# Kernel tuning notes

Hardware: AMD Instinct MI355X
Metric: run time of the kernel (lower is better)

The kernel has to match this reference:

```python
import jax, jax.numpy as jnp
import numpy as np

NUM_HEADS = 4
WS = 3


def setup_inputs() -> dict:
    key = jax.random.key(0)
    k1, k2, k3 = jax.random.split(key, 3)
    B, Hs, Ws_, C = 16, 96, 96, 256
    x = jax.random.normal(k1, (B, Hs * Ws_, C), dtype=jnp.float32)
    # torch nn.Linear weights: [out_features, in_features]
    Wqkv = jax.random.normal(k2, (3 * C, C), dtype=jnp.float32) * (1.0 / np.sqrt(C))
    Wproj = jax.random.normal(k3, (C, C), dtype=jnp.float32) * (1.0 / np.sqrt(C))
    return {"x": x, "Wqkv": Wqkv, "Wproj": Wproj, "H": Hs, "W": Ws_}


def reference(x, Wqkv, Wproj, H, W):
    B, N, C = x.shape
    ws = WS
    nh = NUM_HEADS
    hd = C // nh
    scale = hd ** -0.5

    pad_h = (ws - H % ws) % ws
    pad_w = (ws - W % ws) % ws
    xg = x.reshape(B, H, W, C)
    if pad_h > 0 or pad_w > 0:
        xg = jnp.pad(xg, ((0, 0), (0, pad_h), (0, pad_w), (0, 0)))
    H_pad, W_pad = H + pad_h, W + pad_w
    nWh, nWw = H_pad // ws, W_pad // ws
    Bw = B * nWh * nWw

    # window partition: [B, nWh, ws, nWw, ws, C] -> [Bw, ws*ws, C]
    xw = xg.reshape(B, nWh, ws, nWw, ws, C).transpose(0, 1, 3, 2, 4, 5)
    xw = xw.reshape(Bw, ws * ws, C)

    # qkv projection (Linear, no bias): x @ W^T
    qkv = xw @ Wqkv.T                                   # [Bw, 9, 3C]
    qkv = qkv.reshape(Bw, ws * ws, 3, nh, hd).transpose(2, 0, 3, 1, 4)
    q, k, v = qkv[0], qkv[1], qkv[2]                    # [Bw, nh, 9, hd]

    attn = jnp.einsum("bhqd,bhkd->bhqk", q, k) * scale  # [Bw, nh, 9, 9]
    attn = jax.nn.softmax(attn, axis=-1)
    out = jnp.einsum("bhqk,bhkd->bhqd", attn, v)        # [Bw, nh, 9, hd]
    out = out.transpose(0, 2, 1, 3).reshape(Bw, ws * ws, C)
    out = out @ Wproj.T

    # window unpartition
    out = out.reshape(B, nWh, nWw, ws, ws, C).transpose(0, 1, 3, 2, 4, 5)
    out = out.reshape(B, H_pad, W_pad, C)
    if pad_h > 0 or pad_w > 0:
        out = out[:, :H, :W, :]
    return out.reshape(B, H * W, C)
```

## Files before the change

kernel.cpp:

```cpp
#include <hip/hip_runtime.h>
#include <hip/hip_bf16.h>

using f32x4  = __attribute__((ext_vector_type(4))) float;
using bf16x8 = __attribute__((ext_vector_type(8))) short;
using bf16x4 = __attribute__((ext_vector_type(4))) short;
using u32x2  = __attribute__((ext_vector_type(2))) unsigned int;
using u32x4  = __attribute__((ext_vector_type(4))) unsigned int;

__device__ __forceinline__ float bf2f(short s) {
    unsigned u = ((unsigned)(unsigned short)s) << 16;
    return __builtin_bit_cast(float, u);
}
__device__ __forceinline__ unsigned short f2b(float f) {
    unsigned u = __builtin_bit_cast(unsigned, f);
    unsigned r = u + 0x7FFFu + ((u >> 16) & 1u);
    return (unsigned short)(r >> 16);
}
__device__ __forceinline__ void gl_lds16(const void* g, void* l) {
    __builtin_amdgcn_global_load_lds((const __attribute__((address_space(1))) void*)g,
                                     (__attribute__((address_space(3))) void*)l, 16, 0, 0);
}

__global__ void k_wconv(const float* __restrict__ wq, const float* __restrict__ wp,
                        unsigned short* __restrict__ out) {
    int i = blockIdx.x * 256 + threadIdx.x;
    float v = (i < 196608) ? wq[i] : wp[i - 196608];
    out[i] = f2b(v);
}

__global__ __launch_bounds__(256) void k_qkv2(
    const float* __restrict__ x,
    const unsigned short* __restrict__ wqkv,
    unsigned short* __restrict__ qkv)
{
    __shared__ unsigned short As[128 * 256];
    __shared__ unsigned short Bs[128 * 64];
    const int tid = threadIdx.x;
    const int wv = tid >> 6, ln = tid & 63;
    const int lr = ln & 15, lk = ln >> 4;
    const int l8 = ln >> 3, c8 = ln & 7;

    const int b = blockIdx.x;
    const int w = (b & 7) * 144 + (b >> 3);
    const size_t m0 = (size_t)w * 128;
    const int mq = (wv >> 1) * 64, nq = (wv & 1) * 64;

#pragma unroll
    for (int i = 0; i < 16; ++i) {
        int idx = tid + 256 * i;
        int row = idx >> 5, ch = idx & 31;
        const f32x4* p = (const f32x4*)(x + (m0 + row) * 256 + ch * 8);
        f32x4 f0 = p[0], f1 = p[1];
        bf16x8 v;
#pragma unroll
        for (int j = 0; j < 4; ++j) {
            v[j]     = (short)f2b(f0[j]);
            v[4 + j] = (short)f2b(f1[j]);
        }
        *(bf16x8*)&As[row * 256 + (ch ^ (row & 7)) * 8] = v;
    }
    __syncthreads();

#pragma unroll 1
    for (int nc = 0; nc < 6; ++nc) {
        const int n0 = nc * 128;
        f32x4 acc[4][4];
#pragma unroll
        for (int mi = 0; mi < 4; ++mi)
#pragma unroll
            for (int ni = 0; ni < 4; ++ni) {
                f32x4 z = {0.f, 0.f, 0.f, 0.f};
                acc[mi][ni] = z;
            }

#pragma unroll 1
        for (int ks = 0; ks < 4; ++ks) {
            __syncthreads();
#pragma unroll
            for (int i = 0; i < 4; ++i) {
                int r8 = i * 8 + l8;
                int sc = (c8 ^ (r8 & 7)) * 8;
                gl_lds16(wqkv + (size_t)(n0 + wv * 32 + r8) * 256 + ks * 64 + sc,
                         &Bs[(wv * 32 + i * 8) * 64]);
            }
            __syncthreads();

#pragma unroll
            for (int kk = 0; kk < 2; ++kk) {
                bf16x8 av[4], bv[4];
#pragma unroll
                for (int i = 0; i < 4; ++i) {
                    int ar = mq + i * 16 + lr;
                    int ch = ks * 8 + kk * 4 + lk;
                    av[i] = *(const bf16x8*)&As[ar * 256 + ((ch ^ (ar & 7)) * 8)];
                    int br = nq + i * 16 + lr;
                    bv[i] = *(const bf16x8*)&Bs[br * 64 + (((kk * 4 + lk) ^ (br & 7)) * 8)];
                }
#pragma unroll
                for (int mi = 0; mi < 4; ++mi)
#pragma unroll
                    for (int ni = 0; ni < 4; ++ni)
                        acc[mi][ni] = __builtin_amdgcn_mfma_f32_16x16x32_bf16(bv[ni], av[mi], acc[mi][ni], 0, 0, 0);
            }
        }

#pragma unroll
        for (int mi = 0; mi < 4; ++mi) {
            const size_t row = m0 + mq + mi * 16 + lr;
#pragma unroll
            for (int ni = 0; ni < 4; ++ni) {
                u32x2 u;
                u[0] = (unsigned)f2b(acc[mi][ni][0]) | ((unsigned)f2b(acc[mi][ni][1]) << 16);
                u[1] = (unsigned)f2b(acc[mi][ni][2]) | ((unsigned)f2b(acc[mi][ni][3]) << 16);
                *(u32x2*)(qkv + row * 768 + n0 + nq + ni * 16 + lk * 4) = u;
            }
        }
    }
}

__global__ __launch_bounds__(256) void k_attn(
    unsigned short* __restrict__ qkv)
{
    constexpr int LQ = 68;
    __shared__ unsigned short Ks[144 * LQ];
    __shared__ unsigned short Vs[144 * LQ];
    const int tid = threadIdx.x;
    const int t3 = blockIdx.x;
    const int hf = blockIdx.y;
    const int h  = blockIdx.z;
    const int bb = t3 >> 5, wh = t3 & 31;

    for (int idx = tid; idx < 1152; idx += 256) {
        int row = idx >> 3, ch = idx & 7;
        int ww = row / 9, t = row - ww * 9;
        int rr = t / 3, cc = t - rr * 3;
        size_t xrow = (size_t)bb * 9216 + (wh * 3 + rr) * 96 + hf * 48 + ww * 3 + cc;
        *(bf16x8*)&Ks[row * LQ + ch * 8] = *(const bf16x8*)(qkv + xrow * 768 + 256 + h * 64 + ch * 8);
        *(bf16x8*)&Vs[row * LQ + ch * 8] = *(const bf16x8*)(qkv + xrow * 768 + 512 + h * 64 + ch * 8);
    }
    __syncthreads();

#pragma unroll 1
    for (int pass = 0; pass < 2; ++pass) {
        int row;
        bool act;
        if (pass == 0) { row = tid >> 1;            act = true; }
        else           { row = 128 + (tid >> 1);    act = tid < 32; }
        if (act) {
            const int hc = tid & 1;
            const int w9 = (row / 9) * 9;
            int t = row - w9;
            int rr = t / 3, cc = t - rr * 3;
            size_t xrow = (size_t)bb * 9216 + (wh * 3 + rr) * 96 + hf * 48 + (w9 / 9) * 3 + cc;
            unsigned short* qp = qkv + xrow * 768 + h * 64 + hc * 32;
            float q[32];
#pragma unroll
            for (int g = 0; g < 4; ++g) {
                bf16x8 v = *(const bf16x8*)(qp + g * 8);
#pragma unroll
                for (int j = 0; j < 8; ++j) q[g * 8 + j] = bf2f(v[j]);
            }
            float s[9];
#pragma unroll
            for (int kk = 0; kk < 9; ++kk) {
                float acc = 0.f;
#pragma unroll
                for (int g = 0; g < 4; ++g) {
                    bf16x8 v = *(const bf16x8*)&Ks[(w9 + kk) * LQ + hc * 32 + g * 8];
#pragma unroll
                    for (int j = 0; j < 8; ++j) acc += q[g * 8 + j] * bf2f(v[j]);
                }
                s[kk] = acc;
            }
#pragma unroll
            for (int kk = 0; kk < 9; ++kk)
                s[kk] = (s[kk] + __shfl_xor(s[kk], 1)) * 0.125f;
            float m = s[0];
#pragma unroll
            for (int kk = 1; kk < 9; ++kk) m = fmaxf(m, s[kk]);
            float sum = 0.f;
#pragma unroll
            for (int kk = 0; kk < 9; ++kk) { s[kk] = __expf(s[kk] - m); sum += s[kk]; }
            float inv = 1.f / sum;
            float o[32];
#pragma unroll
            for (int d = 0; d < 32; ++d) o[d] = 0.f;
#pragma unroll
            for (int kk = 0; kk < 9; ++kk) {
                float pk = s[kk] * inv;
#pragma unroll
                for (int g = 0; g < 4; ++g) {
                    bf16x8 v = *(const bf16x8*)&Vs[(w9 + kk) * LQ + hc * 32 + g * 8];
#pragma unroll
                    for (int j = 0; j < 8; ++j) o[g * 8 + j] += pk * bf2f(v[j]);
                }
            }
#pragma unroll
            for (int grp = 0; grp < 4; ++grp) {
                u32x4 u;
#pragma unroll
                for (int e = 0; e < 4; ++e) {
                    int i0 = grp * 8 + e * 2;
                    u[e] = (unsigned)f2b(o[i0]) | ((unsigned)f2b(o[i0 + 1]) << 16);
                }
                *(u32x4*)(qp + grp * 8) = u;
            }
        }
    }
}

__global__ __launch_bounds__(256) void k_proj(
    const unsigned short* __restrict__ ain,
    const unsigned short* __restrict__ wproj,
    float* __restrict__ out)
{
    __shared__ unsigned short As[128 * 64];
    __shared__ unsigned short Bs[128 * 64];
    const int tid = threadIdx.x;
    const int wv = tid >> 6, ln = tid & 63;
    const int lr = ln & 15, lk = ln >> 4;
    const int l8 = ln >> 3, c8 = ln & 7;

    int b = blockIdx.x;
    int w = (b & 7) * 288 + (b >> 3);
    const int n0 = (w / 1152) * 128;
    const int m0 = (w % 1152) * 128;
    const int mq = (wv >> 1) * 64, nq = (wv & 1) * 64;

    f32x4 acc[4][4];
#pragma unroll
    for (int mi = 0; mi < 4; ++mi)
#pragma unroll
        for (int ni = 0; ni < 4; ++ni) {
            f32x4 z = {0.f, 0.f, 0.f, 0.f};
            acc[mi][ni] = z;
        }

#pragma unroll 1
    for (int ks = 0; ks < 4; ++ks) {
        const int k0 = ks * 64;
        __syncthreads();
#pragma unroll
        for (int i = 0; i < 4; ++i) {
            int r8 = i * 8 + l8;
            int sc = (c8 ^ (r8 & 7)) * 8;
            gl_lds16(ain   + (size_t)(m0 + wv * 32 + r8) * 768 + k0 + sc,
                     &As[(wv * 32 + i * 8) * 64]);
            gl_lds16(wproj + (size_t)(n0 + wv * 32 + r8) * 256 + k0 + sc,
                     &Bs[(wv * 32 + i * 8) * 64]);
        }
        __syncthreads();

#pragma unroll
        for (int kk = 0; kk < 2; ++kk) {
            bf16x8 av[4], bv[4];
#pragma unroll
            for (int i = 0; i < 4; ++i) {
                int ar = mq + i * 16 + lr;
                av[i] = *(const bf16x8*)&As[ar * 64 + (((kk * 4 + lk) ^ (ar & 7)) * 8)];
                int br = nq + i * 16 + lr;
                bv[i] = *(const bf16x8*)&Bs[br * 64 + (((kk * 4 + lk) ^ (br & 7)) * 8)];
            }
#pragma unroll
            for (int mi = 0; mi < 4; ++mi)
#pragma unroll
                for (int ni = 0; ni < 4; ++ni)
                    acc[mi][ni] = __builtin_amdgcn_mfma_f32_16x16x32_bf16(bv[ni], av[mi], acc[mi][ni], 0, 0, 0);
        }
    }

#pragma unroll
    for (int mi = 0; mi < 4; ++mi) {
        const size_t row = m0 + mq + mi * 16 + lr;
#pragma unroll
        for (int ni = 0; ni < 4; ++ni)
            *(f32x4*)&out[row * 256 + n0 + nq + ni * 16 + lk * 4] = acc[mi][ni];
    }
}


__device__ __forceinline__ int grow_of(int wbase, int row) {
    int wi = row / 9;
    int t  = row - wi * 9;
    int w  = wbase + wi;
    if (w >= 16384) return -1;
    int b = w >> 10, rem = w & 1023;
    int wh = rem >> 5, ww = rem & 31;
    int r = t / 3, c = t - r * 3;
    return b * 9216 + (wh * 3 + r) * 96 + ww * 3 + c;
}

__global__ __launch_bounds__(256) void k_winattn_fb(
    const float* __restrict__ x,
    const unsigned short* __restrict__ wqkv,
    unsigned short* __restrict__ aout)
{
    constexpr int LDA = 264;
    constexpr int LQ  = 68;
    __shared__ unsigned short As[64 * LDA];
    __shared__ unsigned short Qb[3][64 * LQ];
    __shared__ int rowmap[64];

    const int tid = threadIdx.x;
    const int wbase = blockIdx.x * 7;
    const int wv = tid >> 6, ln = tid & 63;
    const int lr = ln & 15, lk = ln >> 4;
    const int mw = wv >> 1, nw = wv & 1;

    if (tid < 64)
        rowmap[tid] = (tid < 63) ? grow_of(wbase, tid) : -1;
    __syncthreads();

    for (int idx = tid; idx < 64 * 32; idx += 256) {
        int row = idx >> 5, g = idx & 31;
        int gr = rowmap[row];
        bf16x8 v;
        if (gr >= 0) {
            const f32x4* p = (const f32x4*)(x + (size_t)gr * 256 + g * 8);
            f32x4 f0 = p[0], f1 = p[1];
#pragma unroll
            for (int j = 0; j < 4; ++j) {
                v[j]     = (short)f2b(f0[j]);
                v[4 + j] = (short)f2b(f1[j]);
            }
        } else {
#pragma unroll
            for (int j = 0; j < 8; ++j) v[j] = 0;
        }
        *(bf16x8*)&As[row * LDA + g * 8] = v;
    }
    __syncthreads();

#pragma unroll 1
    for (int h = 0; h < 4; ++h) {
#pragma unroll 1
        for (int part = 0; part < 3; ++part) {
            const int j0 = part * 256 + h * 64 + nw * 32;
            bf16x8 w[2][8];
#pragma unroll
            for (int ni = 0; ni < 2; ++ni)
#pragma unroll
                for (int kk = 0; kk < 8; ++kk)
                    w[ni][kk] = *(const bf16x8*)(wqkv + (size_t)(j0 + ni * 16 + lr) * 256 + kk * 32 + lk * 8);

            f32x4 acc[2][2];
#pragma unroll
            for (int mi = 0; mi < 2; ++mi)
#pragma unroll
                for (int ni = 0; ni < 2; ++ni) {
                    f32x4 z = {0.f, 0.f, 0.f, 0.f};
                    acc[mi][ni] = z;
                }
#pragma unroll
            for (int kk = 0; kk < 8; ++kk) {
                const int k0 = kk * 32 + lk * 8;
                bf16x8 a0 = *(const bf16x8*)&As[(mw * 32 + lr) * LDA + k0];
                bf16x8 a1 = *(const bf16x8*)&As[(mw * 32 + 16 + lr) * LDA + k0];
                acc[0][0] = __builtin_amdgcn_mfma_f32_16x16x32_bf16(w[0][kk], a0, acc[0][0], 0, 0, 0);
                acc[1][0] = __builtin_amdgcn_mfma_f32_16x16x32_bf16(w[0][kk], a1, acc[1][0], 0, 0, 0);
                acc[0][1] = __builtin_amdgcn_mfma_f32_16x16x32_bf16(w[1][kk], a0, acc[0][1], 0, 0, 0);
                acc[1][1] = __builtin_amdgcn_mfma_f32_16x16x32_bf16(w[1][kk], a1, acc[1][1], 0, 0, 0);
            }
#pragma unroll
            for (int mi = 0; mi < 2; ++mi)
#pragma unroll
                for (int ni = 0; ni < 2; ++ni) {
                    int row = mw * 32 + mi * 16 + lr;
                    int col = nw * 32 + ni * 16 + lk * 4;
                    u32x2 u;
                    u[0] = (unsigned)f2b(acc[mi][ni][0]) | ((unsigned)f2b(acc[mi][ni][1]) << 16);
                    u[1] = (unsigned)f2b(acc[mi][ni][2]) | ((unsigned)f2b(acc[mi][ni][3]) << 16);
                    *(u32x2*)&Qb[part][row * LQ + col] = u;
                }
        }
        __syncthreads();
        {
            const int row = wv * 16 + lr;
            const int c   = lk;
            if (row < 63) {
                const int w9 = (row / 9) * 9;
                float q[16];
#pragma unroll
                for (int g = 0; g < 4; ++g) {
                    bf16x4 v = *(const bf16x4*)&Qb[0][row * LQ + c * 16 + g * 4];
#pragma unroll
                    for (int j = 0; j < 4; ++j) q[g * 4 + j] = bf2f(v[j]);
                }
                float s[9];
#pragma unroll
                for (int kk = 0; kk < 9; ++kk) {
                    float t = 0.f;
#pragma unroll
                    for (int g = 0; g < 4; ++g) {
                        bf16x4 v = *(const bf16x4*)&Qb[1][(w9 + kk) * LQ + c * 16 + g * 4];
#pragma unroll
                        for (int j = 0; j < 4; ++j) t += q[g * 4 + j] * bf2f(v[j]);
                    }
                    s[kk] = t;
                }
#pragma unroll
                for (int kk = 0; kk < 9; ++kk) {
                    float t = s[kk];
                    t += __shfl_xor(t, 16);
                    t += __shfl_xor(t, 32);
                    s[kk] = t * 0.125f;
                }
                float m = s[0];
#pragma unroll
                for (int kk = 1; kk < 9; ++kk) m = fmaxf(m, s[kk]);
                float sum = 0.f;
#pragma unroll
                for (int kk = 0; kk < 9; ++kk) { s[kk] = __expf(s[kk] - m); sum += s[kk]; }
                float inv = 1.f / sum;
                float o[16];
#pragma unroll
                for (int d = 0; d < 16; ++d) o[d] = 0.f;
#pragma unroll
                for (int kk = 0; kk < 9; ++kk) {
                    float pk = s[kk] * inv;
#pragma unroll
                    for (int g = 0; g < 4; ++g) {
                        bf16x4 v = *(const bf16x4*)&Qb[2][(w9 + kk) * LQ + c * 16 + g * 4];
#pragma unroll
                        for (int j = 0; j < 4; ++j) o[g * 4 + j] += pk * bf2f(v[j]);
                    }
                }
                const int gr = rowmap[row];
                if (gr >= 0) {
#pragma unroll
                    for (int half = 0; half < 2; ++half) {
                        u32x4 u;
#pragma unroll
                        for (int e = 0; e < 4; ++e) {
                            int i0 = half * 8 + e * 2;
                            u[e] = (unsigned)f2b(o[i0]) | ((unsigned)f2b(o[i0 + 1]) << 16);
                        }
                        *(u32x4*)(aout + (size_t)gr * 256 + h * 64 + c * 16 + half * 8) = u;
                    }
                }
            }
        }
        __syncthreads();
    }
}

__global__ __launch_bounds__(256) void k_proj_fb(
    const unsigned short* __restrict__ ain,
    const unsigned short* __restrict__ wproj,
    float* __restrict__ out)
{
    const int tid = threadIdx.x;
    const int wv = tid >> 6, ln = tid & 63;
    const int lr = ln & 15, lk = ln >> 4;
    const size_t row0 = (size_t)blockIdx.x * 128;

    bf16x8 af[2][8];
#pragma unroll
    for (int mi = 0; mi < 2; ++mi) {
        const size_t row = row0 + wv * 32 + mi * 16 + lr;
#pragma unroll
        for (int kk = 0; kk < 8; ++kk)
            af[mi][kk] = *(const bf16x8*)(ain + row * 256 + kk * 32 + lk * 8);
    }
#pragma unroll
    for (int nc = 0; nc < 4; ++nc) {
        const int j0 = nc * 64;
        f32x4 acc[2][4];
#pragma unroll
        for (int mi = 0; mi < 2; ++mi)
#pragma unroll
            for (int ni = 0; ni < 4; ++ni) {
                f32x4 z = {0.f, 0.f, 0.f, 0.f};
                acc[mi][ni] = z;
            }
#pragma unroll
        for (int kk = 0; kk < 8; ++kk) {
            bf16x8 w[4];
#pragma unroll
            for (int ni = 0; ni < 4; ++ni)
                w[ni] = *(const bf16x8*)(wproj + (size_t)(j0 + ni * 16 + lr) * 256 + kk * 32 + lk * 8);
#pragma unroll
            for (int ni = 0; ni < 4; ++ni) {
                acc[0][ni] = __builtin_amdgcn_mfma_f32_16x16x32_bf16(w[ni], af[0][kk], acc[0][ni], 0, 0, 0);
                acc[1][ni] = __builtin_amdgcn_mfma_f32_16x16x32_bf16(w[ni], af[1][kk], acc[1][ni], 0, 0, 0);
            }
        }
#pragma unroll
        for (int mi = 0; mi < 2; ++mi) {
            const size_t row = row0 + wv * 32 + mi * 16 + lr;
#pragma unroll
            for (int ni = 0; ni < 4; ++ni)
                *(f32x4*)&out[row * 256 + j0 + ni * 16 + lk * 4] = acc[mi][ni];
        }
    }
}

extern "C" void kernel_launch(void* const* d_in, const int* in_sizes, int n_in,
                              void* d_out, int out_size, void* d_ws, size_t ws_size,
                              hipStream_t stream) {
    const float* x  = (const float*)d_in[0];
    const float* wq = (const float*)d_in[1];
    const float* wp = (const float*)d_in[2];
    unsigned short* wsb     = (unsigned short*)d_ws;
    unsigned short* wqkv_b  = wsb;
    unsigned short* wproj_b = wsb + 196608;
    float* out = (float*)d_out;

    k_wconv<<<1024, 256, 0, stream>>>(wq, wp, wsb);

    const size_t need = 524288ULL + 147456ULL * 768ULL * 2ULL;
    if (ws_size >= need) {
        unsigned short* qkv = wsb + 262144;
        k_qkv2<<<1152, 256, 0, stream>>>(x, wqkv_b, qkv);
        k_attn<<<dim3(512, 2, 4), 256, 0, stream>>>(qkv);
        k_proj<<<2304, 256, 0, stream>>>(qkv, wproj_b, out);
    } else {
        unsigned short* aout = wsb + 262144;
        k_winattn_fb<<<2341, 256, 0, stream>>>(x, wqkv_b, aout);
        k_proj_fb  <<<1152, 256, 0, stream>>>(aout, wproj_b, out);
    }
}
```

Baseline: 300.3 us.

## Split QKV GEMM into per-N-tile blocks with streamed K tiles of x

The QKV projection kernel no longer stages a full 128x256 bf16 x tile in LDS and loops over six N chunks. Each block now computes a single 128x128 output tile and streams 64-wide K slices of x, converting fp32 to bf16 on the fly. This cuts LDS use and launches 6x more blocks with a min-occupancy hint, aiming for more concurrent waves. The cost is that x is read and converted six times instead of once. The proj kernel's tile order is also changed so that the two N tiles sharing an M tile are adjacent, improving L2 reuse of the attention output.

```diff
diff --git a/kernel.cpp b/kernel.cpp
--- a/kernel.cpp
+++ b/kernel.cpp
@@ -28,12 +28,12 @@
     out[i] = f2b(v);
 }
 
-__global__ __launch_bounds__(256) void k_qkv2(
+__global__ __launch_bounds__(256, 3) void k_qkv3(
     const float* __restrict__ x,
     const unsigned short* __restrict__ wqkv,
     unsigned short* __restrict__ qkv)
 {
-    __shared__ unsigned short As[128 * 256];
+    __shared__ unsigned short As[128 * 64];
     __shared__ unsigned short Bs[128 * 64];
     const int tid = threadIdx.x;
     const int wv = tid >> 6, ln = tid & 63;
@@ -41,79 +41,74 @@
     const int l8 = ln >> 3, c8 = ln & 7;
 
     const int b = blockIdx.x;
-    const int w = (b & 7) * 144 + (b >> 3);
-    const size_t m0 = (size_t)w * 128;
+    const int w = (b & 7) * 864 + (b >> 3);
+    const size_t m0 = (size_t)(w / 6) * 128;
+    const int n0 = (w % 6) * 128;
     const int mq = (wv >> 1) * 64, nq = (wv & 1) * 64;
 
-#pragma unroll
-    for (int i = 0; i < 16; ++i) {
-        int idx = tid + 256 * i;
-        int row = idx >> 5, ch = idx & 31;
-        const f32x4* p = (const f32x4*)(x + (m0 + row) * 256 + ch * 8);
-        f32x4 f0 = p[0], f1 = p[1];
-        bf16x8 v;
-#pragma unroll
-        for (int j = 0; j < 4; ++j) {
-            v[j]     = (short)f2b(f0[j]);
-            v[4 + j] = (short)f2b(f1[j]);
-        }
-        *(bf16x8*)&As[row * 256 + (ch ^ (row & 7)) * 8] = v;
-    }
-    __syncthreads();
+    f32x4 acc[4][4];
+#pragma unroll
+    for (int mi = 0; mi < 4; ++mi)
+#pragma unroll
+        for (int ni = 0; ni < 4; ++ni) {
+            f32x4 z = {0.f, 0.f, 0.f, 0.f};
+            acc[mi][ni] = z;
+        }
 
 #pragma unroll 1
-    for (int nc = 0; nc < 6; ++nc) {
-        const int n0 = nc * 128;
-        f32x4 acc[4][4];
-#pragma unroll
-        for (int mi = 0; mi < 4; ++mi)
-#pragma unroll
-            for (int ni = 0; ni < 4; ++ni) {
-                f32x4 z = {0.f, 0.f, 0.f, 0.f};
-                acc[mi][ni] = z;
-            }
-
-#pragma unroll 1
-        for (int ks = 0; ks < 4; ++ks) {
-            __syncthreads();
+    for (int ks = 0; ks < 4; ++ks) {
+        const int k0 = ks * 64;
+        __syncthreads();
+#pragma unroll
+        for (int i = 0; i < 4; ++i) {
+            int r8 = i * 8 + l8;
+            int sc = (c8 ^ (r8 & 7)) * 8;
+            gl_lds16(wqkv + (size_t)(n0 + wv * 32 + r8) * 256 + k0 + sc,
+                     &Bs[(wv * 32 + i * 8) * 64]);
+        }
+#pragma unroll
+        for (int i = 0; i < 4; ++i) {
+            int slot = tid + 256 * i;
+            int row = slot >> 3, ch = slot & 7;
+            const f32x4* p = (const f32x4*)(x + (m0 + row) * 256 + k0 + ch * 8);
+            f32x4 f0 = p[0], f1 = p[1];
+            bf16x8 v;
+#pragma unroll
+            for (int j = 0; j < 4; ++j) {
+                v[j]     = (short)f2b(f0[j]);
+                v[4 + j] = (short)f2b(f1[j]);
+            }
+            *(bf16x8*)&As[row * 64 + ((ch ^ (row & 7)) * 8)] = v;
+        }
+        __syncthreads();
+
+#pragma unroll
+        for (int kk = 0; kk < 2; ++kk) {
+            bf16x8 av[4], bv[4];
 #pragma unroll
             for (int i = 0; i < 4; ++i) {
-                int r8 = i * 8 + l8;
-                int sc = (c8 ^ (r8 & 7)) * 8;
-                gl_lds16(wqkv + (size_t)(n0 + wv * 32 + r8) * 256 + ks * 64 + sc,
-                         &Bs[(wv * 32 + i * 8) * 64]);
-            }
-            __syncthreads();
-
-#pragma unroll
-            for (int kk = 0; kk < 2; ++kk) {
-                bf16x8 av[4], bv[4];
-#pragma unroll
-                for (int i = 0; i < 4; ++i) {
-                    int ar = mq + i * 16 + lr;
-                    int ch = ks * 8 + kk * 4 + lk;
-                    av[i] = *(const bf16x8*)&As[ar * 256 + ((ch ^ (ar & 7)) * 8)];
-                    int br = nq + i * 16 + lr;
-                    bv[i] = *(const bf16x8*)&Bs[br * 64 + (((kk * 4 + lk) ^ (br & 7)) * 8)];
-                }
-#pragma unroll
-                for (int mi = 0; mi < 4; ++mi)
-#pragma unroll
-                    for (int ni = 0; ni < 4; ++ni)
-                        acc[mi][ni] = __builtin_amdgcn_mfma_f32_16x16x32_bf16(bv[ni], av[mi], acc[mi][ni], 0, 0, 0);
-            }
-        }
-
-#pragma unroll
-        for (int mi = 0; mi < 4; ++mi) {
-            const size_t row = m0 + mq + mi * 16 + lr;
-#pragma unroll
-            for (int ni = 0; ni < 4; ++ni) {
-                u32x2 u;
-                u[0] = (unsigned)f2b(acc[mi][ni][0]) | ((unsigned)f2b(acc[mi][ni][1]) << 16);
-                u[1] = (unsigned)f2b(acc[mi][ni][2]) | ((unsigned)f2b(acc[mi][ni][3]) << 16);
-                *(u32x2*)(qkv + row * 768 + n0 + nq + ni * 16 + lk * 4) = u;
-            }
+                int ar = mq + i * 16 + lr;
+                av[i] = *(const bf16x8*)&As[ar * 64 + (((kk * 4 + lk) ^ (ar & 7)) * 8)];
+                int br = nq + i * 16 + lr;
+                bv[i] = *(const bf16x8*)&Bs[br * 64 + (((kk * 4 + lk) ^ (br & 7)) * 8)];
+            }
+#pragma unroll
+            for (int mi = 0; mi < 4; ++mi)
+#pragma unroll
+                for (int ni = 0; ni < 4; ++ni)
+                    acc[mi][ni] = __builtin_amdgcn_mfma_f32_16x16x32_bf16(bv[ni], av[mi], acc[mi][ni], 0, 0, 0);
+        }
+    }
+
+#pragma unroll
+    for (int mi = 0; mi < 4; ++mi) {
+        const size_t row = m0 + mq + mi * 16 + lr;
+#pragma unroll
+        for (int ni = 0; ni < 4; ++ni) {
+            u32x2 u;
+            u[0] = (unsigned)f2b(acc[mi][ni][0]) | ((unsigned)f2b(acc[mi][ni][1]) << 16);
+            u[1] = (unsigned)f2b(acc[mi][ni][2]) | ((unsigned)f2b(acc[mi][ni][3]) << 16);
+            *(u32x2*)(qkv + row * 768 + n0 + nq + ni * 16 + lk * 4) = u;
         }
     }
 }
@@ -223,8 +218,8 @@
 
     int b = blockIdx.x;
     int w = (b & 7) * 288 + (b >> 3);
-    const int n0 = (w / 1152) * 128;
-    const int m0 = (w % 1152) * 128;
+    const size_t m0 = (size_t)(w >> 1) * 128;
+    const int n0 = (w & 1) * 128;
     const int mq = (wv >> 1) * 64, nq = (wv & 1) * 64;
 
     f32x4 acc[4][4];
@@ -244,7 +239,7 @@
         for (int i = 0; i < 4; ++i) {
             int r8 = i * 8 + l8;
             int sc = (c8 ^ (r8 & 7)) * 8;
-            gl_lds16(ain   + (size_t)(m0 + wv * 32 + r8) * 768 + k0 + sc,
+            gl_lds16(ain   + (m0 + wv * 32 + r8) * 768 + k0 + sc,
                      &As[(wv * 32 + i * 8) * 64]);
             gl_lds16(wproj + (size_t)(n0 + wv * 32 + r8) * 256 + k0 + sc,
                      &Bs[(wv * 32 + i * 8) * 64]);
@@ -511,7 +506,7 @@
     const size_t need = 524288ULL + 147456ULL * 768ULL * 2ULL;
     if (ws_size >= need) {
         unsigned short* qkv = wsb + 262144;
-        k_qkv2<<<1152, 256, 0, stream>>>(x, wqkv_b, qkv);
+        k_qkv3<<<6912, 256, 0, stream>>>(x, wqkv_b, qkv);
         k_attn<<<dim3(512, 2, 4), 256, 0, stream>>>(qkv);
         k_proj<<<2304, 256, 0, stream>>>(qkv, wproj_b, out);
     } else {
```

New measurement: 285.7 us. 1.05x faster.
